# Kernel tuning notes

Hardware: AMD Instinct MI355X
Metric: run time of the kernel (lower is better)

Reference implementation:

```python
import jax, jax.numpy as jnp
import numpy as np

V, E, S, B, N, H = 32000, 1024, 1024, 4, 4, 16
DH = E // H
DFF = 4 * E
EPS = 1e-6


def _sinusoidal_pe(max_len, d):
    pos = np.arange(max_len)[:, None].astype(np.float32)
    div = np.power(10000.0, np.arange(0, d, 2).astype(np.float32) / d)
    pe = np.zeros((max_len, d), dtype=np.float32)
    pe[:, 0::2] = np.sin(pos / div)
    pe[:, 1::2] = np.cos(pos / div)
    return jnp.asarray(pe)


def layer_norm(x, g, b):
    mu = jnp.mean(x, axis=-1, keepdims=True)
    var = jnp.var(x, axis=-1, keepdims=True)
    return (x - mu) * jax.lax.rsqrt(var + EPS) * g + b


def setup_inputs() -> dict:
    key = jax.random.key(0)
    ks = iter(jax.random.split(key, 32))
    s = 0.02
    d = {}
    d['tokens'] = jax.random.randint(next(ks), (B, S), 0, V)
    d['emb'] = jax.random.normal(next(ks), (V, E), jnp.float32) * s
    d['pe'] = _sinusoidal_pe(S, E)
    # stacked per-layer params, leading dim N
    for name, shape in [('Wq', (N, E, E)), ('Wk', (N, E, E)), ('Wv', (N, E, E)), ('Wo', (N, E, E)),
                        ('W1', (N, E, DFF)), ('W2', (N, DFF, E))]:
        d[name] = jax.random.normal(next(ks), shape, jnp.float32) * s
    for name, shape in [('bq', (N, E)), ('bk', (N, E)), ('bv', (N, E)), ('bo', (N, E)),
                        ('b1', (N, DFF)), ('b2', (N, E))]:
        d[name] = jnp.zeros(shape, jnp.float32)
    d['ln1_g'] = jnp.ones((N, E)); d['ln1_b'] = jnp.zeros((N, E))
    d['ln2_g'] = jnp.ones((N, E)); d['ln2_b'] = jnp.zeros((N, E))
    d['enc_g'] = jnp.ones((E,)); d['enc_b'] = jnp.zeros((E,))
    d['fin_g'] = jnp.ones((E,)); d['fin_b'] = jnp.zeros((E,))
    d['Wout'] = jax.random.normal(next(ks), (E, V), jnp.float32) * s
    d['bout'] = jnp.zeros((V,), jnp.float32)
    return d


def _mha(x, Wq, bq, Wk, bk, Wv, bv, Wo, bo):
    b, s, _ = x.shape
    q = (x @ Wq + bq).reshape(b, s, H, DH)
    k = (x @ Wk + bk).reshape(b, s, H, DH)
    v = (x @ Wv + bv).reshape(b, s, H, DH)
    scores = jnp.einsum('bqhd,bkhd->bhqk', q, k) / jnp.sqrt(jnp.float32(DH))
    attn = jax.nn.softmax(scores, axis=-1)
    out = jnp.einsum('bhqk,bkhd->bqhd', attn, v).reshape(b, s, E)
    return out @ Wo + bo


def reference(tokens, emb, pe, Wq, bq, Wk, bk, Wv, bv, Wo, bo,
              W1, b1, W2, b2, ln1_g, ln1_b, ln2_g, ln2_b,
              enc_g, enc_b, fin_g, fin_b, Wout, bout):
    x = emb[tokens] + pe[None, :tokens.shape[1]]  # [B,S,E]; dropout = identity (eval)
    for i in range(N):
        # sublayer 0: x + LN(MHA(x))  (source's unusual residual order)
        a = _mha(x, Wq[i], bq[i], Wk[i], bk[i], Wv[i], bv[i], Wo[i], bo[i])
        x = x + layer_norm(a, ln1_g[i], ln1_b[i])
        # sublayer 1: x + LN(FF(x))
        f = jax.nn.relu(x @ W1[i] + b1[i]) @ W2[i] + b2[i]
        x = x + layer_norm(f, ln2_g[i], ln2_b[i])
    x = layer_norm(x, enc_g, enc_b)      # encoder final LN
    x = layer_norm(x, fin_g, fin_b)      # Transformer-level LN
    return x @ Wout + bout               # [B,S,V]
```

## Files before the change

### kernel.cpp

```cpp
#include <hip/hip_runtime.h>
#include <hip/hip_bf16.h>
#include <stdint.h>

#define EDIM 1024
#define DFFDIM 4096
#define NLAYER 4
#define BATCH 4
#define SEQ 1024
#define NHEAD 16
#define DHEAD 64
#define VOCAB 32000
#define MROWS (BATCH*SEQ)
#define QKVLD (3*EDIM)
#define EPSF 1e-6f

typedef float f32x4 __attribute__((ext_vector_type(4)));
typedef short s16x8 __attribute__((ext_vector_type(8)));
typedef __bf16 bf16x8 __attribute__((ext_vector_type(8)));

__device__ inline unsigned short f2bf(float f) {
  union { float f; uint32_t u; } v; v.f = f;
  uint32_t r = v.u + 0x7fffu + ((v.u >> 16) & 1u);
  return (unsigned short)(r >> 16);
}

__device__ __forceinline__ void gload16(const void* g, void* l) {
  __builtin_amdgcn_global_load_lds(
      (const __attribute__((address_space(1))) void*)g,
      (__attribute__((address_space(3))) void*)l, 16, 0, 0);
}

__global__ __launch_bounds__(256) void embed_kernel(
    const int* __restrict__ tokens, const float* __restrict__ emb,
    const float* __restrict__ pe, float* __restrict__ x,
    unsigned short* __restrict__ xb) {
  const int row = blockIdx.x;
  const int s = row & (SEQ - 1);
  const int tok = tokens[row];
  const int c = threadIdx.x * 4;
  float4 ev = *(const float4*)(emb + (size_t)tok * EDIM + c);
  float4 pv = *(const float4*)(pe + (size_t)s * EDIM + c);
  float4 o;
  o.x = ev.x + pv.x; o.y = ev.y + pv.y; o.z = ev.z + pv.z; o.w = ev.w + pv.w;
  *(float4*)(x + (size_t)row * EDIM + c) = o;
  unsigned short* xr = xb + (size_t)row * EDIM + c;
  xr[0] = f2bf(o.x); xr[1] = f2bf(o.y); xr[2] = f2bf(o.z); xr[3] = f2bf(o.w);
}

__global__ __launch_bounds__(256) void transpose_w(
    const float* __restrict__ src, unsigned short* __restrict__ dst,
    int N, int K) {
  __shared__ float tl[64][65];
  const int t = threadIdx.x;
  const int k0 = blockIdx.x * 64, n0 = blockIdx.y * 64;
  const int c = (t & 15) * 4, r0 = t >> 4;
  #pragma unroll
  for (int i = 0; i < 4; ++i) {
    const int r = r0 + i * 16;
    float4 v = *(const float4*)(src + (size_t)(k0 + r) * N + n0 + c);
    tl[r][c] = v.x; tl[r][c + 1] = v.y; tl[r][c + 2] = v.z; tl[r][c + 3] = v.w;
  }
  __syncthreads();
  #pragma unroll
  for (int i = 0; i < 4; ++i) {
    const int n = r0 + i * 16;
    uint2 o;
    o.x = (uint32_t)f2bf(tl[c + 0][n]) | ((uint32_t)f2bf(tl[c + 1][n]) << 16);
    o.y = (uint32_t)f2bf(tl[c + 2][n]) | ((uint32_t)f2bf(tl[c + 3][n]) << 16);
    *(uint2*)(dst + (size_t)(n0 + n) * K + k0 + c) = o;
  }
}

__global__ __launch_bounds__(256) void pack_bias(
    const float* __restrict__ bq, const float* __restrict__ bk,
    const float* __restrict__ bv, float* __restrict__ dst) {
  const int idx = blockIdx.x * 256 + threadIdx.x;
  if (idx >= NLAYER * QKVLD) return;
  const int layer = idx / QKVLD, c = idx % QKVLD;
  float v;
  if (c < 1024)      v = bq[layer * 1024 + c];
  else if (c < 2048) v = bk[layer * 1024 + c - 1024];
  else               v = bv[layer * 1024 + c - 2048];
  dst[idx] = v;
}

template<int BM, int OUT_BF16, int RELU>
__global__ __launch_bounds__(BM * 2, (BM == 256) ? 2 : 3) void gemm3(
    const unsigned short* __restrict__ A, const unsigned short* __restrict__ Bt,
    const float* __restrict__ bias, void* __restrict__ Cout,
    int Nld, int K, int NBLK) {
  constexpr int BUFB = BM * 128;
  constexpr int ABYTES = BM * 64;
  constexpr int WN = (BM == 256) ? 4 : 2;
  constexpr int MF = BM / 32;
  __shared__ __attribute__((aligned(16))) char smb[3 * BUFB];
  const int t = threadIdx.x, lane = t & 63;
  const int wave = t >> 6;
  const int wr = wave / WN, wc = wave % WN;
  const int l15 = lane & 15, lg = lane >> 4;

  const int cpx = gridDim.x >> 3;
  const int bid = blockIdx.x;
  const int swz = (bid & 7) * cpx + (bid >> 3);
  const int m0 = (swz / NBLK) * BM;
  const int n0 = (swz % NBLK) * BM;

  f32x4 acc[MF][4];
  #pragma unroll
  for (int i = 0; i < MF; ++i)
    #pragma unroll
    for (int j = 0; j < 4; ++j)
      acc[i][j] = (f32x4){0.f, 0.f, 0.f, 0.f};

  const int srow = t >> 2;
  const int scol = (((t & 3) ^ ((t >> 3) & 3)) << 3);
  const unsigned short* agp = A  + (size_t)(m0 + srow) * K + scol;
  const unsigned short* bgp = Bt + (size_t)(n0 + srow) * K + scol;
  const size_t rhalf = (size_t)(BM / 2) * K;

  const int cxo = (lg * 16) ^ (((l15 >> 1) & 3) << 4);
  const int rdA = (wr * (BM / 2) + l15) * 64 + cxo;
  const int rdB = ABYTES + (wc * 64 + l15) * 64 + cxo;

  auto stage_tile = [&](int b, int kt) {
    const int k0 = kt * 32;
    char* d = smb + b * BUFB + t * 16;
    gload16(agp + k0, d);
    gload16(agp + rhalf + k0, d + BM * 32);
    gload16(bgp + k0, d + ABYTES);
    gload16(bgp + rhalf + k0, d + ABYTES + BM * 32);
  };

  const int NT = K / 32;
  stage_tile(0, 0);
  stage_tile(1, 1);
  asm volatile("s_waitcnt vmcnt(4)" ::: "memory");
  __builtin_amdgcn_s_barrier();
  __builtin_amdgcn_sched_barrier(0);

  int bufc = 0, bufn = 2;
  for (int tt = 0; tt < NT; ++tt) {
    if (tt + 2 < NT) stage_tile(bufn, tt + 2);

    const char* ab = smb + bufc * BUFB;
    bf16x8 af[MF], bf[4];
    #pragma unroll
    for (int mf = 0; mf < MF; ++mf)
      af[mf] = *(const bf16x8*)(ab + rdA + mf * 1024);
    #pragma unroll
    for (int nf = 0; nf < 4; ++nf)
      bf[nf] = *(const bf16x8*)(ab + rdB + nf * 1024);

    __builtin_amdgcn_s_setprio(1);
    #pragma unroll
    for (int mf = 0; mf < MF; ++mf)
      #pragma unroll
      for (int nf = 0; nf < 4; ++nf)
        acc[mf][nf] = __builtin_amdgcn_mfma_f32_16x16x32_bf16(af[mf], bf[nf], acc[mf][nf], 0, 0, 0);
    __builtin_amdgcn_s_setprio(0);

    if (tt + 2 < NT)      asm volatile("s_waitcnt vmcnt(4)" ::: "memory");
    else if (tt + 1 < NT) asm volatile("s_waitcnt vmcnt(0)" ::: "memory");
    __builtin_amdgcn_sched_barrier(0);
    __builtin_amdgcn_s_barrier();
    __builtin_amdgcn_sched_barrier(0);

    bufc = (bufc == 2) ? 0 : bufc + 1;
    bufn = (bufn == 2) ? 0 : bufn + 1;
  }

  #pragma unroll
  for (int mf = 0; mf < MF; ++mf) {
    #pragma unroll
    for (int nf = 0; nf < 4; ++nf) {
      const int col = n0 + wc * 64 + nf * 16 + l15;
      const float bv = bias[col];
      #pragma unroll
      for (int r = 0; r < 4; ++r) {
        const int row = m0 + wr * (BM / 2) + mf * 16 + lg * 4 + r;
        float val = acc[mf][nf][r] + bv;
        if (RELU) val = fmaxf(val, 0.f);
        if (OUT_BF16)
          ((unsigned short*)Cout)[(size_t)row * Nld + col] = f2bf(val);
        else
          ((float*)Cout)[(size_t)row * Nld + col] = val;
      }
    }
  }
}

__global__ __launch_bounds__(256) void attn_kernel(
    const unsigned short* __restrict__ qkv, unsigned short* __restrict__ ctx) {
  const int b = blockIdx.z, h = blockIdx.y;
  const int t = threadIdx.x, wave = t >> 6, lane = t & 63;
  const int l15 = lane & 15, lg = lane >> 4;
  const int qrow0 = blockIdx.x * 64 + wave * 16;
  const unsigned short* qbs = qkv + (size_t)b * SEQ * QKVLD + h * DHEAD;
  const unsigned short* kbs = qbs + EDIM;
  const unsigned short* vbs = qbs + 2 * EDIM;
  __shared__ unsigned short Ksm[64][72];
  __shared__ unsigned short VTs[64 * 64];
  __shared__ unsigned short p_lds[4][16][72];

  const unsigned short* qp = qbs + (size_t)(qrow0 + l15) * QKVLD + lg * 8;
  bf16x8 a0 = *(const bf16x8*)qp;
  bf16x8 a1 = *(const bf16x8*)(qp + 32);

  f32x4 o0 = {0,0,0,0}, o1 = {0,0,0,0}, o2 = {0,0,0,0}, o3 = {0,0,0,0};
  float m[4], ls[4];
  #pragma unroll
  for (int r = 0; r < 4; ++r) { m[r] = -1e30f; ls[r] = 0.f; }

  const int sr = t >> 2;
  const int sc = (t & 3) * 16;
  const unsigned short* kgp = kbs + (size_t)sr * QKVLD + sc;
  const unsigned short* vgp = vbs + (size_t)sr * QKVLD + sc;
  const size_t tilestep = (size_t)64 * QKVLD;

  s16x8 kr0 = *(const s16x8*)kgp, kr1 = *(const s16x8*)(kgp + 8);
  s16x8 vr0 = *(const s16x8*)vgp, vr1 = *(const s16x8*)(vgp + 8);

  const int NT = SEQ / 64;
  for (int j = 0; j < NT; ++j) {
    *(s16x8*)&Ksm[sr][sc] = kr0;
    *(s16x8*)&Ksm[sr][sc + 8] = kr1;
    #pragma unroll
    for (int c = 0; c < 2; ++c) {
      s16x8 vv = c ? vr1 : vr0;
      #pragma unroll
      for (int e = 0; e < 8; ++e) {
        const int d = sc + c * 8 + e;
        const int byteo = d * 128 + ((sr * 2) ^ (e << 4));
        *(unsigned short*)((char*)VTs + byteo) = (unsigned short)vv[e];
      }
    }
    __syncthreads();

    f32x4 s[4];
    __builtin_amdgcn_s_setprio(1);
    #pragma unroll
    for (int g = 0; g < 4; ++g) {
      bf16x8 k0 = *(const bf16x8*)&Ksm[g * 16 + l15][lg * 8];
      bf16x8 k1 = *(const bf16x8*)&Ksm[g * 16 + l15][32 + lg * 8];
      f32x4 z = {0, 0, 0, 0};
      z = __builtin_amdgcn_mfma_f32_16x16x32_bf16(a0, k0, z, 0, 0, 0);
      s[g] = __builtin_amdgcn_mfma_f32_16x16x32_bf16(a1, k1, z, 0, 0, 0);
    }
    __builtin_amdgcn_s_setprio(0);

    if (j + 1 < NT) {
      const unsigned short* kn = kgp + (size_t)(j + 1) * tilestep;
      const unsigned short* vn = vgp + (size_t)(j + 1) * tilestep;
      kr0 = *(const s16x8*)kn; kr1 = *(const s16x8*)(kn + 8);
      vr0 = *(const s16x8*)vn; vr1 = *(const s16x8*)(vn + 8);
    }

    float mx[4], scl[4], rs[4];
    #pragma unroll
    for (int g = 0; g < 4; ++g)
      #pragma unroll
      for (int r = 0; r < 4; ++r) s[g][r] *= 0.125f;
    #pragma unroll
    for (int r = 0; r < 4; ++r)
      mx[r] = fmaxf(fmaxf(s[0][r], s[1][r]), fmaxf(s[2][r], s[3][r]));
    #pragma unroll
    for (int off = 1; off < 16; off <<= 1) {
      #pragma unroll
      for (int r = 0; r < 4; ++r) mx[r] = fmaxf(mx[r], __shfl_xor(mx[r], off));
    }
    #pragma unroll
    for (int r = 0; r < 4; ++r) {
      const float mn = fmaxf(m[r], mx[r]);
      scl[r] = __expf(m[r] - mn);
      m[r] = mn;
    }
    #pragma unroll
    for (int g = 0; g < 4; ++g)
      #pragma unroll
      for (int r = 0; r < 4; ++r) s[g][r] = __expf(s[g][r] - m[r]);
    #pragma unroll
    for (int r = 0; r < 4; ++r)
      rs[r] = (s[0][r] + s[1][r]) + (s[2][r] + s[3][r]);
    #pragma unroll
    for (int off = 1; off < 16; off <<= 1) {
      #pragma unroll
      for (int r = 0; r < 4; ++r) rs[r] += __shfl_xor(rs[r], off);
    }
    #pragma unroll
    for (int r = 0; r < 4; ++r) {
      ls[r] = ls[r] * scl[r] + rs[r];
      o0[r] *= scl[r]; o1[r] *= scl[r]; o2[r] *= scl[r]; o3[r] *= scl[r];
      #pragma unroll
      for (int g = 0; g < 4; ++g)
        p_lds[wave][lg * 4 + r][g * 16 + l15] = f2bf(s[g][r]);
    }
    bf16x8 pa0 = *(const bf16x8*)&p_lds[wave][l15][lg * 8];
    bf16x8 pa1 = *(const bf16x8*)&p_lds[wave][l15][32 + lg * 8];

    auto vld = [&](int dg, int c) {
      const int byteo = (dg * 16 + l15) * 128 + ((c * 64 + lg * 16) ^ ((l15 & 7) << 4));
      return *(const bf16x8*)((const char*)VTs + byteo);
    };
    __builtin_amdgcn_s_setprio(1);
    o0 = __builtin_amdgcn_mfma_f32_16x16x32_bf16(pa0, vld(0, 0), o0, 0, 0, 0);
    o1 = __builtin_amdgcn_mfma_f32_16x16x32_bf16(pa0, vld(1, 0), o1, 0, 0, 0);
    o2 = __builtin_amdgcn_mfma_f32_16x16x32_bf16(pa0, vld(2, 0), o2, 0, 0, 0);
    o3 = __builtin_amdgcn_mfma_f32_16x16x32_bf16(pa0, vld(3, 0), o3, 0, 0, 0);
    o0 = __builtin_amdgcn_mfma_f32_16x16x32_bf16(pa1, vld(0, 1), o0, 0, 0, 0);
    o1 = __builtin_amdgcn_mfma_f32_16x16x32_bf16(pa1, vld(1, 1), o1, 0, 0, 0);
    o2 = __builtin_amdgcn_mfma_f32_16x16x32_bf16(pa1, vld(2, 1), o2, 0, 0, 0);
    o3 = __builtin_amdgcn_mfma_f32_16x16x32_bf16(pa1, vld(3, 1), o3, 0, 0, 0);
    __builtin_amdgcn_s_setprio(0);
    __syncthreads();
  }

  unsigned short* cp = ctx + (size_t)b * SEQ * EDIM + h * DHEAD;
  #pragma unroll
  for (int r = 0; r < 4; ++r) {
    unsigned short* cr = cp + (size_t)(qrow0 + lg * 4 + r) * EDIM;
    const float inv = 1.f / ls[r];
    cr[l15]      = f2bf(o0[r] * inv);
    cr[16 + l15] = f2bf(o1[r] * inv);
    cr[32 + l15] = f2bf(o2[r] * inv);
    cr[48 + l15] = f2bf(o3[r] * inv);
  }
}

__global__ __launch_bounds__(256) void ln_add_kernel(
    const float* __restrict__ a, const float* __restrict__ g, const float* __restrict__ bb,
    float* __restrict__ x, unsigned short* __restrict__ xb) {
  const int row = blockIdx.x, t = threadIdx.x;
  const float* ar = a + (size_t)row * EDIM;
  float4 av = *(const float4*)(ar + t * 4);
  float s = av.x + av.y + av.z + av.w;
  float qq = av.x * av.x + av.y * av.y + av.z * av.z + av.w * av.w;
  #pragma unroll
  for (int off = 1; off < 64; off <<= 1) { s += __shfl_xor(s, off); qq += __shfl_xor(qq, off); }
  __shared__ float red[8];
  const int wv = t >> 6;
  if ((t & 63) == 0) { red[wv] = s; red[4 + wv] = qq; }
  __syncthreads();
  s = red[0] + red[1] + red[2] + red[3];
  qq = red[4] + red[5] + red[6] + red[7];
  const float mean = s * (1.f / EDIM);
  const float rstd = rsqrtf(qq * (1.f / EDIM) - mean * mean + EPSF);
  float4 gv = *(const float4*)(g + t * 4);
  float4 bv = *(const float4*)(bb + t * 4);
  float* xr = x + (size_t)row * EDIM;
  float4 xv = *(float4*)(xr + t * 4);
  float4 o;
  o.x = xv.x + (av.x - mean) * rstd * gv.x + bv.x;
  o.y = xv.y + (av.y - mean) * rstd * gv.y + bv.y;
  o.z = xv.z + (av.z - mean) * rstd * gv.z + bv.z;
  o.w = xv.w + (av.w - mean) * rstd * gv.w + bv.w;
  *(float4*)(xr + t * 4) = o;
  unsigned short* xbr = xb + (size_t)row * EDIM + t * 4;
  xbr[0] = f2bf(o.x); xbr[1] = f2bf(o.y); xbr[2] = f2bf(o.z); xbr[3] = f2bf(o.w);
}

__global__ __launch_bounds__(256) void final_ln_kernel(
    const float* __restrict__ x, const float* __restrict__ g1, const float* __restrict__ b1,
    const float* __restrict__ g2, const float* __restrict__ b2,
    unsigned short* __restrict__ xb) {
  const int row = blockIdx.x, t = threadIdx.x;
  __shared__ float red[8];
  const int wv = t >> 6;
  const float* xr = x + (size_t)row * EDIM;
  float4 v = *(const float4*)(xr + t * 4);

  float s = v.x + v.y + v.z + v.w;
  float qq = v.x * v.x + v.y * v.y + v.z * v.z + v.w * v.w;
  #pragma unroll
  for (int off = 1; off < 64; off <<= 1) { s += __shfl_xor(s, off); qq += __shfl_xor(qq, off); }
  if ((t & 63) == 0) { red[wv] = s; red[4 + wv] = qq; }
  __syncthreads();
  s = red[0] + red[1] + red[2] + red[3];
  qq = red[4] + red[5] + red[6] + red[7];
  __syncthreads();
  float mean = s * (1.f / EDIM);
  float rstd = rsqrtf(qq * (1.f / EDIM) - mean * mean + EPSF);
  float4 g1v = *(const float4*)(g1 + t * 4);
  float4 b1v = *(const float4*)(b1 + t * 4);
  float4 tv;
  tv.x = (v.x - mean) * rstd * g1v.x + b1v.x;
  tv.y = (v.y - mean) * rstd * g1v.y + b1v.y;
  tv.z = (v.z - mean) * rstd * g1v.z + b1v.z;
  tv.w = (v.w - mean) * rstd * g1v.w + b1v.w;

  s = tv.x + tv.y + tv.z + tv.w;
  qq = tv.x * tv.x + tv.y * tv.y + tv.z * tv.z + tv.w * tv.w;
  #pragma unroll
  for (int off = 1; off < 64; off <<= 1) { s += __shfl_xor(s, off); qq += __shfl_xor(qq, off); }
  if ((t & 63) == 0) { red[wv] = s; red[4 + wv] = qq; }
  __syncthreads();
  s = red[0] + red[1] + red[2] + red[3];
  qq = red[4] + red[5] + red[6] + red[7];
  mean = s * (1.f / EDIM);
  rstd = rsqrtf(qq * (1.f / EDIM) - mean * mean + EPSF);
  float4 g2v = *(const float4*)(g2 + t * 4);
  float4 b2v = *(const float4*)(b2 + t * 4);
  unsigned short* o = xb + (size_t)row * EDIM + t * 4;
  o[0] = f2bf((tv.x - mean) * rstd * g2v.x + b2v.x);
  o[1] = f2bf((tv.y - mean) * rstd * g2v.y + b2v.y);
  o[2] = f2bf((tv.z - mean) * rstd * g2v.z + b2v.z);
  o[3] = f2bf((tv.w - mean) * rstd * g2v.w + b2v.w);
}

extern "C" void kernel_launch(void* const* d_in, const int* in_sizes, int n_in,
                              void* d_out, int out_size, void* d_ws, size_t ws_size,
                              hipStream_t stream) {
  const int*   tokens = (const int*)d_in[0];
  const float* emb    = (const float*)d_in[1];
  const float* pe     = (const float*)d_in[2];
  const float* Wq     = (const float*)d_in[3];
  const float* Wk     = (const float*)d_in[4];
  const float* Wv     = (const float*)d_in[5];
  const float* Wo     = (const float*)d_in[6];
  const float* W1     = (const float*)d_in[7];
  const float* W2     = (const float*)d_in[8];
  const float* bq     = (const float*)d_in[9];
  const float* bk     = (const float*)d_in[10];
  const float* bv     = (const float*)d_in[11];
  const float* bo     = (const float*)d_in[12];
  const float* b1     = (const float*)d_in[13];
  const float* b2     = (const float*)d_in[14];
  const float* ln1_g  = (const float*)d_in[15];
  const float* ln1_b  = (const float*)d_in[16];
  const float* ln2_g  = (const float*)d_in[17];
  const float* ln2_b  = (const float*)d_in[18];
  const float* enc_g  = (const float*)d_in[19];
  const float* enc_b  = (const float*)d_in[20];
  const float* fin_g  = (const float*)d_in[21];
  const float* fin_b  = (const float*)d_in[22];
  const float* Wout   = (const float*)d_in[23];
  const float* bout   = (const float*)d_in[24];
  float* out = (float*)d_out;

  uint8_t* p = (uint8_t*)d_ws;
  auto alloc = [&](size_t bytes) {
    void* r = (void*)p;
    p += (bytes + 255) & ~(size_t)255;
    return r;
  };
  float*          x     = (float*)alloc((size_t)MROWS * EDIM * 4);
  unsigned short* xb    = (unsigned short*)alloc((size_t)MROWS * EDIM * 2);
  float*          tbuf  = (float*)alloc((size_t)MROWS * EDIM * 4);
  unsigned short* qkv   = (unsigned short*)alloc((size_t)MROWS * QKVLD * 2);
  unsigned short* ctx   = (unsigned short*)alloc((size_t)MROWS * EDIM * 2);
  unsigned short* wlt   = (unsigned short*)alloc((size_t)NLAYER * 12 * 1024 * 1024 * 2);
  unsigned short* woutt = (unsigned short*)alloc((size_t)VOCAB * EDIM * 2);
  float*          bqkv  = (float*)alloc((size_t)NLAYER * QKVLD * 4);
  unsigned short* ff1   = qkv;
  if ((size_t)(p - (uint8_t*)d_ws) > ws_size) return;

  const dim3 blk(256);
  const dim3 blk512(512);
  const size_t LW = (size_t)12 * 1024 * 1024;
  const size_t M1 = 1024 * 1024;

  for (int i = 0; i < NLAYER; ++i) {
    unsigned short* lb = wlt + (size_t)i * LW;
    transpose_w<<<dim3(16, 16),  blk, 0, stream>>>(Wq + (size_t)i * M1, lb,          1024, 1024);
    transpose_w<<<dim3(16, 16),  blk, 0, stream>>>(Wk + (size_t)i * M1, lb + M1,     1024, 1024);
    transpose_w<<<dim3(16, 16),  blk, 0, stream>>>(Wv + (size_t)i * M1, lb + 2 * M1, 1024, 1024);
    transpose_w<<<dim3(16, 16),  blk, 0, stream>>>(Wo + (size_t)i * M1, lb + 3 * M1, 1024, 1024);
    transpose_w<<<dim3(16, 64),  blk, 0, stream>>>(W1 + (size_t)i * 4 * M1, lb + 4 * M1, 4096, 1024);
    transpose_w<<<dim3(64, 16),  blk, 0, stream>>>(W2 + (size_t)i * 4 * M1, lb + 8 * M1, 1024, 4096);
  }
  transpose_w<<<dim3(16, 500), blk, 0, stream>>>(Wout, woutt, VOCAB, 1024);
  pack_bias<<<(NLAYER * QKVLD + 255) / 256, blk, 0, stream>>>(bq, bk, bv, bqkv);

  embed_kernel<<<MROWS, blk, 0, stream>>>(tokens, emb, pe, x, xb);

  const int MB2 = MROWS / 256;
  const int MB1 = MROWS / 128;
  for (int i = 0; i < NLAYER; ++i) {
    unsigned short* lb = wlt + (size_t)i * LW;
    gemm3<256, 1, 0><<<MB2 * (QKVLD / 256), blk512, 0, stream>>>(
        xb, lb, bqkv + (size_t)i * QKVLD, qkv, QKVLD, EDIM, QKVLD / 256);
    attn_kernel<<<dim3(SEQ / 64, NHEAD, BATCH), blk, 0, stream>>>(qkv, ctx);
    gemm3<128, 0, 0><<<MB1 * (EDIM / 128), blk, 0, stream>>>(
        ctx, lb + 3 * M1, bo + i * EDIM, tbuf, EDIM, EDIM, EDIM / 128);
    ln_add_kernel<<<MROWS, blk, 0, stream>>>(tbuf, ln1_g + i * EDIM, ln1_b + i * EDIM, x, xb);
    gemm3<256, 1, 1><<<MB2 * (DFFDIM / 256), blk512, 0, stream>>>(
        xb, lb + 4 * M1, b1 + i * DFFDIM, ff1, DFFDIM, EDIM, DFFDIM / 256);
    gemm3<128, 0, 0><<<MB1 * (EDIM / 128), blk, 0, stream>>>(
        ff1, lb + 8 * M1, b2 + i * EDIM, tbuf, EDIM, DFFDIM, EDIM / 128);
    ln_add_kernel<<<MROWS, blk, 0, stream>>>(tbuf, ln2_g + i * EDIM, ln2_b + i * EDIM, x, xb);
  }

  final_ln_kernel<<<MROWS, blk, 0, stream>>>(x, enc_g, enc_b, fin_g, fin_b, xb);
  gemm3<256, 0, 0><<<MB2 * (VOCAB / 256), blk512, 0, stream>>>(
      xb, woutt, bout, out, VOCAB, EDIM, VOCAB / 256);
}
```

Before: 1.435 ms.

## Double-buffer GEMM register fragments to overlap LDS reads with MFMA

The GEMM main loop now keeps two sets of register fragments. Each iteration splits its MFMA work in half and issues the wait, barrier and LDS fragment loads for the next tile between the two halves. This is meant to hide LDS read latency behind matrix-core work instead of stalling before every tile's MFMAs. The cost is higher VGPR pressure, and the loop now assumes NT is even.

Result: no change. 1.457 ms (+1.6%).

```diff
diff --git a/kernel.cpp b/kernel.cpp
--- a/kernel.cpp
+++ b/kernel.cpp
@@ -131,42 +131,66 @@
     gload16(bgp + rhalf + k0, d + ABYTES + BM * 32);
   };
 
+  auto ld_frags = [&](int b, bf16x8 (&fa)[MF], bf16x8 (&fb)[4]) {
+    const char* ab = smb + b * BUFB;
+    #pragma unroll
+    for (int mf = 0; mf < MF; ++mf)
+      fa[mf] = *(const bf16x8*)(ab + rdA + mf * 1024);
+    #pragma unroll
+    for (int nf = 0; nf < 4; ++nf)
+      fb[nf] = *(const bf16x8*)(ab + rdB + nf * 1024);
+  };
+
   const int NT = K / 32;
+  bf16x8 fA0[MF], fB0[4], fA1[MF], fB1[4];
+
   stage_tile(0, 0);
   stage_tile(1, 1);
   asm volatile("s_waitcnt vmcnt(4)" ::: "memory");
+  __builtin_amdgcn_sched_barrier(0);
   __builtin_amdgcn_s_barrier();
   __builtin_amdgcn_sched_barrier(0);
-
-  int bufc = 0, bufn = 2;
-  for (int tt = 0; tt < NT; ++tt) {
-    if (tt + 2 < NT) stage_tile(bufn, tt + 2);
-
-    const char* ab = smb + bufc * BUFB;
-    bf16x8 af[MF], bf[4];
-    #pragma unroll
-    for (int mf = 0; mf < MF; ++mf)
-      af[mf] = *(const bf16x8*)(ab + rdA + mf * 1024);
-    #pragma unroll
-    for (int nf = 0; nf < 4; ++nf)
-      bf[nf] = *(const bf16x8*)(ab + rdB + nf * 1024);
+  ld_frags(0, fA0, fB0);
+
+  int bufR = 1, bufS = 2;
+  auto do_iter = [&](bf16x8 (&cA)[MF], bf16x8 (&cB)[4],
+                     bf16x8 (&nA)[MF], bf16x8 (&nB)[4], int tt) {
+    if (tt + 2 < NT) stage_tile(bufS, tt + 2);
+    __builtin_amdgcn_sched_barrier(0);
 
     __builtin_amdgcn_s_setprio(1);
     #pragma unroll
-    for (int mf = 0; mf < MF; ++mf)
+    for (int mf = 0; mf < MF / 2; ++mf)
       #pragma unroll
       for (int nf = 0; nf < 4; ++nf)
-        acc[mf][nf] = __builtin_amdgcn_mfma_f32_16x16x32_bf16(af[mf], bf[nf], acc[mf][nf], 0, 0, 0);
+        acc[mf][nf] = __builtin_amdgcn_mfma_f32_16x16x32_bf16(cA[mf], cB[nf], acc[mf][nf], 0, 0, 0);
     __builtin_amdgcn_s_setprio(0);
 
-    if (tt + 2 < NT)      asm volatile("s_waitcnt vmcnt(4)" ::: "memory");
-    else if (tt + 1 < NT) asm volatile("s_waitcnt vmcnt(0)" ::: "memory");
+    if (tt + 1 < NT) {
+      if (tt + 2 < NT) asm volatile("s_waitcnt vmcnt(4)" ::: "memory");
+      else             asm volatile("s_waitcnt vmcnt(0)" ::: "memory");
+      __builtin_amdgcn_sched_barrier(0);
+      __builtin_amdgcn_s_barrier();
+      __builtin_amdgcn_sched_barrier(0);
+      ld_frags(bufR, nA, nB);
+    }
     __builtin_amdgcn_sched_barrier(0);
-    __builtin_amdgcn_s_barrier();
-    __builtin_amdgcn_sched_barrier(0);
-
-    bufc = (bufc == 2) ? 0 : bufc + 1;
-    bufn = (bufn == 2) ? 0 : bufn + 1;
+
+    __builtin_amdgcn_s_setprio(1);
+    #pragma unroll
+    for (int mf = MF / 2; mf < MF; ++mf)
+      #pragma unroll
+      for (int nf = 0; nf < 4; ++nf)
+        acc[mf][nf] = __builtin_amdgcn_mfma_f32_16x16x32_bf16(cA[mf], cB[nf], acc[mf][nf], 0, 0, 0);
+    __builtin_amdgcn_s_setprio(0);
+
+    bufR = (bufR == 2) ? 0 : bufR + 1;
+    bufS = (bufS == 2) ? 0 : bufS + 1;
+  };
+
+  for (int tt = 0; tt < NT; tt += 2) {
+    do_iter(fA0, fB0, fA1, fB1, tt);
+    do_iter(fA1, fB1, fA0, fB0, tt + 1);
   }
 
   #pragma unroll
```

## Fold softmax scale into Wq, use exp2, lazy rescale, packed bf16 P stores

Applied to the files above, without the earlier changes.

Folds the 1/sqrt(d)·log2(e) factor into the Q weights and bias during the weight transpose, so attention can use raw v_exp_f32 (exp2) without a per-score multiply. Running-max rescaling of the output accumulators is skipped unless some row's max grows by more than 8, which removes most per-tile rescale work. P is converted with v_cvt_pk_bf16_f32 and written as packed 8-byte stores instead of scalar stores. The V-transpose LDS swizzle is also changed. The lazy rescale lets unnormalized exponents reach up to 2^8 and slightly changes rounding.

Result: no change. 1.414 ms (-1.4%).

```diff
diff --git a/kernel.cpp b/kernel.cpp
--- a/kernel.cpp
+++ b/kernel.cpp
@@ -13,6 +13,7 @@
 #define MROWS (BATCH*SEQ)
 #define QKVLD (3*EDIM)
 #define EPSF 1e-6f
+#define ALPHA 0.18033688011112043f
 
 typedef float f32x4 __attribute__((ext_vector_type(4)));
 typedef short s16x8 __attribute__((ext_vector_type(8)));
@@ -22,6 +23,13 @@
   union { float f; uint32_t u; } v; v.f = f;
   uint32_t r = v.u + 0x7fffu + ((v.u >> 16) & 1u);
   return (unsigned short)(r >> 16);
+}
+
+__device__ __forceinline__ float fexp2(float x) {
+  float r; asm("v_exp_f32 %0, %1" : "=v"(r) : "v"(x)); return r;
+}
+__device__ __forceinline__ uint32_t cvtpk(float lo, float hi) {
+  uint32_t r; asm("v_cvt_pk_bf16_f32 %0, %1, %2" : "=v"(r) : "v"(lo), "v"(hi)); return r;
 }
 
 __device__ __forceinline__ void gload16(const void* g, void* l) {
@@ -49,7 +57,7 @@
 
 __global__ __launch_bounds__(256) void transpose_w(
     const float* __restrict__ src, unsigned short* __restrict__ dst,
-    int N, int K) {
+    int N, int K, float scale) {
   __shared__ float tl[64][65];
   const int t = threadIdx.x;
   const int k0 = blockIdx.x * 64, n0 = blockIdx.y * 64;
@@ -65,8 +73,8 @@
   for (int i = 0; i < 4; ++i) {
     const int n = r0 + i * 16;
     uint2 o;
-    o.x = (uint32_t)f2bf(tl[c + 0][n]) | ((uint32_t)f2bf(tl[c + 1][n]) << 16);
-    o.y = (uint32_t)f2bf(tl[c + 2][n]) | ((uint32_t)f2bf(tl[c + 3][n]) << 16);
+    o.x = (uint32_t)f2bf(tl[c + 0][n] * scale) | ((uint32_t)f2bf(tl[c + 1][n] * scale) << 16);
+    o.y = (uint32_t)f2bf(tl[c + 2][n] * scale) | ((uint32_t)f2bf(tl[c + 3][n] * scale) << 16);
     *(uint2*)(dst + (size_t)(n0 + n) * K + k0 + c) = o;
   }
 }
@@ -78,7 +86,7 @@
   if (idx >= NLAYER * QKVLD) return;
   const int layer = idx / QKVLD, c = idx % QKVLD;
   float v;
-  if (c < 1024)      v = bq[layer * 1024 + c];
+  if (c < 1024)      v = bq[layer * 1024 + c] * ALPHA;
   else if (c < 2048) v = bk[layer * 1024 + c - 1024];
   else               v = bv[layer * 1024 + c - 2048];
   dst[idx] = v;
@@ -213,6 +221,7 @@
 
   const int sr = t >> 2;
   const int sc = (t & 3) * 16;
+  const int posw = ((sr & 15) << 2) | (sr >> 4);
   const unsigned short* kgp = kbs + (size_t)sr * QKVLD + sc;
   const unsigned short* vgp = vbs + (size_t)sr * QKVLD + sc;
   const size_t tilestep = (size_t)64 * QKVLD;
@@ -230,7 +239,7 @@
       #pragma unroll
       for (int e = 0; e < 8; ++e) {
         const int d = sc + c * 8 + e;
-        const int byteo = d * 128 + ((sr * 2) ^ (e << 4));
+        const int byteo = d * 128 + ((posw * 2) ^ ((d & 7) << 4));
         *(unsigned short*)((char*)VTs + byteo) = (unsigned short)vv[e];
       }
     }
@@ -255,11 +264,7 @@
       vr0 = *(const s16x8*)vn; vr1 = *(const s16x8*)(vn + 8);
     }
 
-    float mx[4], scl[4], rs[4];
-    #pragma unroll
-    for (int g = 0; g < 4; ++g)
-      #pragma unroll
-      for (int r = 0; r < 4; ++r) s[g][r] *= 0.125f;
+    float mx[4];
     #pragma unroll
     for (int r = 0; r < 4; ++r)
       mx[r] = fmaxf(fmaxf(s[0][r], s[1][r]), fmaxf(s[2][r], s[3][r]));
@@ -268,16 +273,26 @@
       #pragma unroll
       for (int r = 0; r < 4; ++r) mx[r] = fmaxf(mx[r], __shfl_xor(mx[r], off));
     }
-    #pragma unroll
-    for (int r = 0; r < 4; ++r) {
-      const float mn = fmaxf(m[r], mx[r]);
-      scl[r] = __expf(m[r] - mn);
-      m[r] = mn;
+
+    bool need = false;
+    #pragma unroll
+    for (int r = 0; r < 4; ++r) need = need || (mx[r] > m[r] + 8.f);
+    if (__any(need)) {
+      #pragma unroll
+      for (int r = 0; r < 4; ++r) {
+        const float mn = fmaxf(m[r], mx[r]);
+        const float scl = fexp2(m[r] - mn);
+        m[r] = mn;
+        ls[r] *= scl;
+        o0[r] *= scl; o1[r] *= scl; o2[r] *= scl; o3[r] *= scl;
+      }
     }
     #pragma unroll
     for (int g = 0; g < 4; ++g)
       #pragma unroll
-      for (int r = 0; r < 4; ++r) s[g][r] = __expf(s[g][r] - m[r]);
+      for (int r = 0; r < 4; ++r) s[g][r] = fexp2(s[g][r] - m[r]);
+
+    float rs[4];
     #pragma unroll
     for (int r = 0; r < 4; ++r)
       rs[r] = (s[0][r] + s[1][r]) + (s[2][r] + s[3][r]);
@@ -288,11 +303,11 @@
     }
     #pragma unroll
     for (int r = 0; r < 4; ++r) {
-      ls[r] = ls[r] * scl[r] + rs[r];
-      o0[r] *= scl[r]; o1[r] *= scl[r]; o2[r] *= scl[r]; o3[r] *= scl[r];
-      #pragma unroll
-      for (int g = 0; g < 4; ++g)
-        p_lds[wave][lg * 4 + r][g * 16 + l15] = f2bf(s[g][r]);
+      ls[r] += rs[r];
+      uint2 w;
+      w.x = cvtpk(s[0][r], s[1][r]);
+      w.y = cvtpk(s[2][r], s[3][r]);
+      *(uint2*)((char*)&p_lds[wave][lg * 4 + r][0] + l15 * 8) = w;
     }
     bf16x8 pa0 = *(const bf16x8*)&p_lds[wave][l15][lg * 8];
     bf16x8 pa1 = *(const bf16x8*)&p_lds[wave][l15][32 + lg * 8];
@@ -460,14 +475,14 @@
 
   for (int i = 0; i < NLAYER; ++i) {
     unsigned short* lb = wlt + (size_t)i * LW;
-    transpose_w<<<dim3(16, 16),  blk, 0, stream>>>(Wq + (size_t)i * M1, lb,          1024, 1024);
-    transpose_w<<<dim3(16, 16),  blk, 0, stream>>>(Wk + (size_t)i * M1, lb + M1,     1024, 1024);
-    transpose_w<<<dim3(16, 16),  blk, 0, stream>>>(Wv + (size_t)i * M1, lb + 2 * M1, 1024, 1024);
-    transpose_w<<<dim3(16, 16),  blk, 0, stream>>>(Wo + (size_t)i * M1, lb + 3 * M1, 1024, 1024);
-    transpose_w<<<dim3(16, 64),  blk, 0, stream>>>(W1 + (size_t)i * 4 * M1, lb + 4 * M1, 4096, 1024);
-    transpose_w<<<dim3(64, 16),  blk, 0, stream>>>(W2 + (size_t)i * 4 * M1, lb + 8 * M1, 1024, 4096);
-  }
-  transpose_w<<<dim3(16, 500), blk, 0, stream>>>(Wout, woutt, VOCAB, 1024);
+    transpose_w<<<dim3(16, 16),  blk, 0, stream>>>(Wq + (size_t)i * M1, lb,          1024, 1024, ALPHA);
+    transpose_w<<<dim3(16, 16),  blk, 0, stream>>>(Wk + (size_t)i * M1, lb + M1,     1024, 1024, 1.0f);
+    transpose_w<<<dim3(16, 16),  blk, 0, stream>>>(Wv + (size_t)i * M1, lb + 2 * M1, 1024, 1024, 1.0f);
+    transpose_w<<<dim3(16, 16),  blk, 0, stream>>>(Wo + (size_t)i * M1, lb + 3 * M1, 1024, 1024, 1.0f);
+    transpose_w<<<dim3(16, 64),  blk, 0, stream>>>(W1 + (size_t)i * 4 * M1, lb + 4 * M1, 4096, 1024, 1.0f);
+    transpose_w<<<dim3(64, 16),  blk, 0, stream>>>(W2 + (size_t)i * 4 * M1, lb + 8 * M1, 1024, 4096, 1.0f);
+  }
+  transpose_w<<<dim3(16, 500), blk, 0, stream>>>(Wout, woutt, VOCAB, 1024, 1.0f);
   pack_bias<<<(NLAYER * QKVLD + 255) / 256, blk, 0, stream>>>(bq, bk, bv, bqkv);
 
   embed_kernel<<<MROWS, blk, 0, stream>>>(tokens, emb, pe, x, xb);
```
